# Optimization experiments

Measured on AMD Instinct MI355X. Metric: run time of the kernel, lower is better.

The kernel has to match this reference:

```python
import jax, jax.numpy as jnp
import numpy as np

D = 768      # feature_dim
HD = 768     # hidden_dim
NH = 4       # num_heads
B, T1, T2 = 4, 128, 128
LN_EPS = 1e-5

def setup_inputs() -> dict:
    key = jax.random.key(0)
    ks = jax.random.split(key, 12)
    s = 0.02
    return {
        'speech_features': jax.random.normal(ks[0], (B, T1, D), jnp.float32),
        'phoneme_features': jax.random.normal(ks[1], (B, T2, D), jnp.float32),
        # per-head attention MLP: Linear(2D->HD), ReLU, Linear(HD->1); stacked over heads
        'W1': jax.random.normal(ks[2], (NH, 2 * D, HD), jnp.float32) * s,
        'b1': jnp.zeros((NH, HD), jnp.float32),
        'w2': jax.random.normal(ks[3], (NH, HD), jnp.float32) * s,
        'b2': jnp.zeros((NH,), jnp.float32),
        # fusion: Linear(2D->2HD), ReLU, Linear(2HD->D), LayerNorm(D)
        'Wf1': jax.random.normal(ks[4], (2 * D, 2 * HD), jnp.float32) * s,
        'bf1': jnp.zeros((2 * HD,), jnp.float32),
        'Wf2': jax.random.normal(ks[5], (2 * HD, D), jnp.float32) * s,
        'bf2': jnp.zeros((D,), jnp.float32),
        'ln_g': jnp.ones((D,), jnp.float32),
        'ln_b': jnp.zeros((D,), jnp.float32),
    }

def reference(speech_features, phoneme_features, W1, b1, w2, b2, Wf1, bf1, Wf2, bf2, ln_g, ln_b):
    d = speech_features.shape[-1]
    # Decompose Linear(cat([speech_t, phoneme])) = speech@W1[:d] + phoneme@W1[d:] + b1
    Wx, Wy = W1[:, :d, :], W1[:, d:, :]
    sx = jnp.einsum('btd,ndh->nbth', speech_features, Wx)   # [NH,B,T1,HD]
    py = jnp.einsum('bsd,ndh->nbsh', phoneme_features, Wy)  # [NH,B,T2,HD]
    hidden = jax.nn.relu(sx[:, :, :, None, :] + py[:, :, None, :, :]
                         + b1[:, None, None, None, :])      # [NH,B,T1,T2,HD]
    scores = jnp.einsum('nbtsh,nh->nbts', hidden, w2) + b2[:, None, None, None]
    attn = jax.nn.softmax(scores, axis=-1).mean(axis=0)     # [B,T1,T2]
    context = jnp.einsum('bts,bsd->btd', attn, phoneme_features)  # [B,T1,D]
    fused = jnp.concatenate([speech_features, context], axis=-1)  # [B,T1,2D]
    # dropout is identity in eval mode
    h = jax.nn.relu(fused @ Wf1 + bf1)
    out = h @ Wf2 + bf2
    mu = out.mean(axis=-1, keepdims=True)
    var = ((out - mu) ** 2).mean(axis=-1, keepdims=True)
    out = (out - mu) * jax.lax.rsqrt(var + LN_EPS) * ln_g + ln_b
    return out.mean(axis=1)  # [B,D]
```

## Files before the change

kernel.cpp:

```cpp
#include <hip/hip_runtime.h>
#include <cstddef>


#define D_  768
#define HD_ 768
#define NH_ 4
#define B_  4
#define T1_ 128
#define T2_ 128
#define M_  (B_*T1_)
#define LN_EPS_ 1e-5f

typedef unsigned short u16;
typedef unsigned int u32;
typedef _Float16 f16;
typedef _Float16 f16x2 __attribute__((ext_vector_type(2)));
typedef __bf16 bf16x8 __attribute__((ext_vector_type(8)));
typedef float f32x4 __attribute__((ext_vector_type(4)));

__device__ __forceinline__ u16 f2bf(float f) {
    union { float f; unsigned int u; } v; v.f = f;
    unsigned int u = v.u + (0x7FFFu + ((v.u >> 16) & 1u));
    return (u16)(u >> 16);
}
__device__ __forceinline__ u16 f16bits(f16 h) {
    return __builtin_bit_cast(unsigned short, h);
}
__device__ __forceinline__ u32 splat2(u16 h) {
    return (u32)h * 0x10001u;
}
__device__ __forceinline__ u32 pk_add(u32 a, u32 b) {
    u32 d; asm("v_pk_add_f16 %0, %1, %2" : "=v"(d) : "v"(a), "v"(b)); return d;
}
__device__ __forceinline__ u32 pk_max0(u32 a) {
    u32 d; asm("v_pk_max_f16 %0, %1, %2" : "=v"(d) : "v"(a), "v"(0u)); return d;
}
__device__ __forceinline__ u32 pk_fma(u32 a, u32 b, u32 c) {
    u32 d; asm("v_pk_fma_f16 %0, %1, %2, %3" : "=v"(d) : "v"(a), "v"(b), "v"(c)); return d;
}
__device__ __forceinline__ float lo_f(u32 u) {
    f16x2 v = __builtin_bit_cast(f16x2, u); return (float)v.x;
}
__device__ __forceinline__ float hi_f(u32 u) {
    f16x2 v = __builtin_bit_cast(f16x2, u); return (float)v.y;
}

template<bool RELU, int MODE>
__device__ __forceinline__ void gemm_mfma_body(
    const u16* __restrict__ A, int lda,
    const u16* __restrict__ Bt, int ldb,
    const float* __restrict__ bias,
    void* __restrict__ C, int ldc, int K, int m0, int n0)
{
    __shared__ __align__(16) u16 As[64][40];
    __shared__ __align__(16) u16 Bs[64][40];
    __shared__ u16 Ts[MODE == 3 ? 64 : 1][MODE == 3 ? 68 : 1];

    const int tid = threadIdx.x;
    const int row = tid >> 2;
    const int kq  = (tid & 3) << 3;
    const int lane = tid & 63;
    const int w  = tid >> 6;
    const int wr = (w >> 1) << 5;
    const int wc = (w & 1) << 5;
    const int l16 = lane & 15;
    const int lk8 = (lane >> 4) << 3;
    const int r4  = (lane >> 4) << 2;

    const u16* aptr = A + (size_t)(m0 + row) * lda + kq;
    const u16* bptr = Bt + (size_t)(n0 + row) * ldb + kq;

    f32x4 acc00 = {0.f,0.f,0.f,0.f}, acc01 = {0.f,0.f,0.f,0.f};
    f32x4 acc10 = {0.f,0.f,0.f,0.f}, acc11 = {0.f,0.f,0.f,0.f};

    uint4 a_nxt = *(const uint4*)aptr;
    uint4 b_nxt = *(const uint4*)bptr;

    for (int k0 = 0; k0 < K; k0 += 32) {
        __syncthreads();
        *(uint4*)&As[row][kq] = a_nxt;
        *(uint4*)&Bs[row][kq] = b_nxt;
        if (k0 + 32 < K) {
            a_nxt = *(const uint4*)(aptr + k0 + 32);
            b_nxt = *(const uint4*)(bptr + k0 + 32);
        }
        __syncthreads();
        bf16x8 af0 = *(const bf16x8*)&As[wr + l16][lk8];
        bf16x8 af1 = *(const bf16x8*)&As[wr + 16 + l16][lk8];
        bf16x8 bf0 = *(const bf16x8*)&Bs[wc + l16][lk8];
        bf16x8 bf1 = *(const bf16x8*)&Bs[wc + 16 + l16][lk8];
        acc00 = __builtin_amdgcn_mfma_f32_16x16x32_bf16(af0, bf0, acc00, 0, 0, 0);
        acc01 = __builtin_amdgcn_mfma_f32_16x16x32_bf16(af0, bf1, acc01, 0, 0, 0);
        acc10 = __builtin_amdgcn_mfma_f32_16x16x32_bf16(af1, bf0, acc10, 0, 0, 0);
        acc11 = __builtin_amdgcn_mfma_f32_16x16x32_bf16(af1, bf1, acc11, 0, 0, 0);
    }

#define EPI_FRAG(ACC, MF, NF)                                                  \
    {                                                                          \
        const int gcol = n0 + wc + (NF)*16 + l16;                              \
        const float bv = bias ? bias[gcol] : 0.f;                              \
        float v_[4];                                                           \
        _Pragma("unroll")                                                      \
        for (int r = 0; r < 4; r++) {                                          \
            float v = ACC[r] + bv;                                             \
            if (RELU) v = fmaxf(v, 0.f);                                       \
            v_[r] = v;                                                         \
        }                                                                      \
        const int lr0 = wr + (MF)*16 + r4;                                     \
        if (MODE == 3) {                                                       \
            const int lc = wc + (NF)*16 + l16;                                 \
            _Pragma("unroll")                                                  \
            for (int r = 0; r < 4; r++) Ts[lc][lr0 + r] = f16bits((f16)v_[r]); \
        } else {                                                               \
            _Pragma("unroll")                                                  \
            for (int r = 0; r < 4; r++) {                                      \
                const size_t off = (size_t)(m0 + lr0 + r) * ldc + gcol;        \
                if (MODE == 0) ((float*)C)[off] = v_[r];                       \
                else if (MODE == 1) ((u16*)C)[off] = f2bf(v_[r]);              \
                else ((u16*)C)[off] = f16bits((f16)v_[r]);                     \
            }                                                                  \
        }                                                                      \
    }
    EPI_FRAG(acc00, 0, 0) EPI_FRAG(acc01, 0, 1)
    EPI_FRAG(acc10, 1, 0) EPI_FRAG(acc11, 1, 1)
#undef EPI_FRAG

    if (MODE == 3) {
        __syncthreads();
        u16* cb = (u16*)C + (size_t)(m0 >> 7) * (768 * 128) + (m0 & 127);
#pragma unroll
        for (int u = 0; u < 4; u++) {
            const int i = tid + u * 256;
            const int hl = i >> 4;
            const int s4 = (i & 15) << 2;
            ushort4 o;
            o.x = Ts[hl][s4 + 0]; o.y = Ts[hl][s4 + 1];
            o.z = Ts[hl][s4 + 2]; o.w = Ts[hl][s4 + 3];
            *(ushort4*)(cb + (size_t)(n0 + hl) * 128 + s4) = o;
        }
    }
}

__global__ __launch_bounds__(256) void prep_kernel(
    const float* __restrict__ speech, const float* __restrict__ phon,
    const float* __restrict__ W1, const float* __restrict__ Wf1,
    const float* __restrict__ Wf2,
    u16* __restrict__ spb, u16* __restrict__ phb,
    u16* __restrict__ w1t, u16* __restrict__ wf1t, u16* __restrict__ wf2t)
{
    const int tid = threadIdx.x;
    int bid = blockIdx.x;
    if (bid < 768) {
        const bool isp = bid < 384;
        const float* in = isp ? speech : phon;
        u16* outb = isp ? spb : phb;
        const int i = ((isp ? bid : bid - 384) * 256 + tid) * 4;
        float4 v = *(const float4*)(in + i);
        ushort4 o;
        o.x = f2bf(v.x); o.y = f2bf(v.y); o.z = f2bf(v.z); o.w = f2bf(v.w);
        *(ushort4*)(outb + i) = o;
        return;
    }
    bid -= 768;
    const float* in; u16* outp; int tx, ty;
    if (bid < 4608) {
        const int z = bid / 1152, r = bid % 1152;
        tx = r % 24; ty = r / 24;
        in = W1 + (size_t)z * 1536 * 768; outp = w1t + (size_t)z * 768 * 1536;
    } else if (bid < 6912) {
        const int r = bid - 4608;
        tx = r % 48; ty = r / 48;
        in = Wf1; outp = wf1t;
    } else {
        const int r = bid - 6912;
        tx = r % 24; ty = r / 24;
        in = Wf2; outp = wf2t;
    }
    const int C = (bid >= 4608 && bid < 6912) ? 1536 : 768;
    const int c0 = tx * 32, r0 = ty * 32;
    __shared__ float tile[32][33];
    const int tr = tid >> 3, tc = (tid & 7) << 2;
    float4 v = *(const float4*)(in + (size_t)(r0 + tr) * C + c0 + tc);
    tile[tr][tc] = v.x; tile[tr][tc + 1] = v.y; tile[tr][tc + 2] = v.z; tile[tr][tc + 3] = v.w;
    __syncthreads();
    ushort4 o;
    o.x = f2bf(tile[tc + 0][tr]); o.y = f2bf(tile[tc + 1][tr]);
    o.z = f2bf(tile[tc + 2][tr]); o.w = f2bf(tile[tc + 3][tr]);
    *(ushort4*)(outp + (size_t)(c0 + tr) * 1536 + r0 + tc) = o;
}

__global__ __launch_bounds__(256) void gemm_sxpy_kernel(
    const u16* __restrict__ sp, const u16* __restrict__ ph,
    const u16* __restrict__ w1t, const float* __restrict__ b1,
    u16* __restrict__ sxf, u16* __restrict__ pyt)
{
    const int z = blockIdx.z;
    const int n = z & 3;
    const bool ispy = z >= 4;
    const u16* Bt = w1t + (size_t)n * 768 * 1536 + (ispy ? 768 : 0);
    if (!ispy) {
        gemm_mfma_body<false, 2>(sp, 768, Bt, 1536, b1 + n * HD_,
                                 sxf + (size_t)n * M_ * HD_, HD_, 768,
                                 blockIdx.y * 64, blockIdx.x * 64);
    } else {
        gemm_mfma_body<false, 3>(ph, 768, Bt, 1536, nullptr,
                                 pyt + (size_t)n * 4 * 768 * 128, 0, 768,
                                 blockIdx.y * 64, blockIdx.x * 64);
    }
}

template<bool RELU, int MODE>
__global__ __launch_bounds__(256) void gemm_mfma_kernel(
    const u16* __restrict__ A, int lda,
    const u16* __restrict__ Bt, int ldb,
    const float* __restrict__ bias,
    void* __restrict__ C, int ldc, int K)
{
    gemm_mfma_body<RELU, MODE>(A, lda, Bt, ldb, bias, C, ldc, K,
                               blockIdx.y * 64, blockIdx.x * 64);
}

__global__ __launch_bounds__(256) void scores_softmax_kernel(
    const u16* __restrict__ sxf,
    const u16* __restrict__ pyt,
    const float* __restrict__ w2,
    float* __restrict__ probs)
{
    const int bid = blockIdx.x;
    const int n = bid >> 6, b = (bid >> 4) & 3, t0 = (bid & 15) * 8;
    const int tid = threadIdx.x, lane = tid & 63, w = tid >> 6;

    __shared__ __align__(16) u32 sxs[8][768];
    __shared__ __align__(16) u32 w2s[768];

    for (int q = 0; q < 6; q++) {
        const int u = tid + q * 256;
        const int r = u / 192;
        const int h4 = (u % 192) * 4;
        ushort4 v = *(const ushort4*)(sxf + ((size_t)(n * 512 + b * 128 + t0 + r)) * 768 + h4);
        sxs[r][h4 + 0] = splat2(v.x);
        sxs[r][h4 + 1] = splat2(v.y);
        sxs[r][h4 + 2] = splat2(v.z);
        sxs[r][h4 + 3] = splat2(v.w);
    }
    for (int q = 0; q < 3; q++) {
        const int i = tid + q * 256;
        w2s[i] = splat2(f16bits((f16)w2[n * 768 + i]));
    }
    __syncthreads();

    const u32* pypanel = (const u32*)(pyt + ((size_t)((n << 2) | b)) * 768 * 128) + lane;

    float accA0 = 0.f, accA1 = 0.f, accB0 = 0.f, accB1 = 0.f;
    const int rA = 2 * w, rB = 2 * w + 1;

    u32 b0[16], b1[16];
#pragma unroll
    for (int j = 0; j < 16; j++) b0[j] = pypanel[(size_t)j * 64];
#pragma unroll
    for (int j = 0; j < 16; j++) b1[j] = pypanel[(size_t)(16 + j) * 64];

    auto compute = [&](const u32 (&buf)[16], int hbase) {
        u32 aA = 0u, aB = 0u;
#pragma unroll
        for (int j = 0; j < 16; j++) {
            const u32 p = buf[j];
            const u32 wj = w2s[hbase + j];
            aA = pk_fma(pk_max0(pk_add(sxs[rA][hbase + j], p)), wj, aA);
            aB = pk_fma(pk_max0(pk_add(sxs[rB][hbase + j], p)), wj, aB);
        }
        accA0 += lo_f(aA); accA1 += hi_f(aA);
        accB0 += lo_f(aB); accB1 += hi_f(aB);
    };

    for (int hc = 0; hc < 768; hc += 32) {
        compute(b0, hc);
        if (hc + 32 < 768) {
#pragma unroll
            for (int j = 0; j < 16; j++) b0[j] = pypanel[(size_t)(hc + 32 + j) * 64];
        }
        compute(b1, hc + 16);
        if (hc + 48 < 768) {
#pragma unroll
            for (int j = 0; j < 16; j++) b1[j] = pypanel[(size_t)(hc + 48 + j) * 64];
        }
    }

#pragma unroll
    for (int which = 0; which < 2; which++) {
        const float s0 = which ? accB0 : accA0;
        const float s1 = which ? accB1 : accA1;
        const int t = t0 + 2 * w + which;
        float mx = fmaxf(s0, s1);
#pragma unroll
        for (int off = 32; off; off >>= 1) mx = fmaxf(mx, __shfl_xor(mx, off, 64));
        const float e0 = expf(s0 - mx), e1 = expf(s1 - mx);
        float sm = e0 + e1;
#pragma unroll
        for (int off = 32; off; off >>= 1) sm += __shfl_xor(sm, off, 64);
        const float inv = 0.25f / sm;
        float2 pr; pr.x = e0 * inv; pr.y = e1 * inv;
        *(float2*)&probs[((size_t)(n * 512 + b * 128 + t)) * 128 + 2 * lane] = pr;
    }
}

__global__ __launch_bounds__(256) void context_fused_kernel(
    const float* __restrict__ probs, const float* __restrict__ phon,
    const float* __restrict__ speech, u16* __restrict__ fused)
{
    const int m = blockIdx.x;
    const int b = m >> 7;
    const int tid = threadIdx.x;
    __shared__ float attn[T2_];
    if (tid < T2_) {
        float a = 0.f;
#pragma unroll
        for (int n = 0; n < NH_; n++)
            a += probs[(size_t)(n * M_ + m) * T2_ + tid];
        attn[tid] = a;
    }
    __syncthreads();
    const float* ph = phon + (size_t)b * T2_ * D_;
#pragma unroll
    for (int j = 0; j < 3; j++) {
        const int d = tid + 256 * j;
        float acc = 0.f;
#pragma unroll 8
        for (int s = 0; s < T2_; s++)
            acc = fmaf(attn[s], ph[(size_t)s * D_ + d], acc);
        fused[(size_t)m * (2 * D_) + d] = f2bf(speech[(size_t)m * D_ + d]);
        fused[(size_t)m * (2 * D_) + D_ + d] = f2bf(acc);
    }
}

__global__ __launch_bounds__(256) void ln_fused_kernel(
    const float* __restrict__ x, const float* __restrict__ g,
    const float* __restrict__ lb, float* __restrict__ out)
{
    const int b = blockIdx.x, tid = threadIdx.x, lane = tid & 63, w = tid >> 6;
    __shared__ float rs[T1_];
    __shared__ float Sred[4];

    float prsum = 0.f;
    for (int i = 0; i < 32; i++) {
        const int row = w * 32 + i;
        const float4* x4 = (const float4*)(x + ((size_t)(b * T1_ + row)) * D_);
        float s = 0.f, ss = 0.f;
#pragma unroll
        for (int j = 0; j < 3; j++) {
            float4 v = x4[j * 64 + lane];
            s += v.x + v.y + v.z + v.w;
            ss += v.x * v.x + v.y * v.y + v.z * v.z + v.w * v.w;
        }
#pragma unroll
        for (int off = 32; off; off >>= 1) {
            s += __shfl_xor(s, off, 64);
            ss += __shfl_xor(ss, off, 64);
        }
        if (lane == 0) {
            const float mu = s * (1.f / D_);
            const float var = ss * (1.f / D_) - mu * mu;
            const float r = rsqrtf(var + LN_EPS_);
            rs[row] = r;
            prsum += mu * r;
        }
    }
    if (lane == 0) Sred[w] = prsum;
    __syncthreads();
    const float S = Sred[0] + Sred[1] + Sred[2] + Sred[3];
    const float* xb = x + (size_t)b * T1_ * D_;
#pragma unroll
    for (int j = 0; j < 3; j++) {
        const int d = tid + 256 * j;
        float acc = 0.f;
#pragma unroll 8
        for (int t = 0; t < T1_; t++)
            acc = fmaf(xb[(size_t)t * D_ + d], rs[t], acc);
        out[b * D_ + d] = g[d] * (acc - S) * (1.f / T1_) + lb[d];
    }
}

extern "C" void kernel_launch(void* const* d_in, const int* in_sizes, int n_in,
                              void* d_out, int out_size, void* d_ws, size_t ws_size,
                              hipStream_t stream)
{
    const float* speech = (const float*)d_in[0];
    const float* phon   = (const float*)d_in[1];
    const float* W1     = (const float*)d_in[2];
    const float* b1     = (const float*)d_in[3];
    const float* w2     = (const float*)d_in[4];
    const float* Wf1    = (const float*)d_in[6];
    const float* bf1    = (const float*)d_in[7];
    const float* Wf2    = (const float*)d_in[8];
    const float* bf2    = (const float*)d_in[9];
    const float* ln_g   = (const float*)d_in[10];
    const float* ln_b   = (const float*)d_in[11];
    float* out = (float*)d_out;

    char* w = (char*)d_ws;
    auto alloc = [&](size_t bytes) { char* p = w; w += (bytes + 1023) & ~(size_t)1023; return p; };
    u16* sp_bf  = (u16*)alloc((size_t)M_ * D_ * 2);
    u16* ph_bf  = (u16*)alloc((size_t)M_ * D_ * 2);
    u16* w1t    = (u16*)alloc((size_t)NH_ * 768 * 1536 * 2);
    u16* wf1t   = (u16*)alloc((size_t)1536 * 1536 * 2);
    u16* wf2t   = (u16*)alloc((size_t)768 * 1536 * 2);
    u16* sxf    = (u16*)alloc((size_t)NH_ * M_ * HD_ * 2);
    u16* pyt    = (u16*)alloc((size_t)NH_ * B_ * 768 * 128 * 2);
    float* probs  = (float*)alloc((size_t)NH_ * M_ * T2_ * 4);
    u16* fusedb = (u16*)alloc((size_t)M_ * 2 * D_ * 2);
    u16* hbuf   = (u16*)alloc((size_t)M_ * 2 * HD_ * 2);
    float* outpre = (float*)alloc((size_t)M_ * D_ * 4);

    hipLaunchKernelGGL(prep_kernel, dim3(8832), dim3(256), 0, stream,
                       speech, phon, W1, Wf1, Wf2, sp_bf, ph_bf, w1t, wf1t, wf2t);
    hipLaunchKernelGGL(gemm_sxpy_kernel, dim3(HD_ / 64, M_ / 64, 8), dim3(256), 0, stream,
                       sp_bf, ph_bf, w1t, b1, sxf, pyt);
    hipLaunchKernelGGL(scores_softmax_kernel, dim3(256), dim3(256), 0, stream,
                       sxf, pyt, w2, probs);
    hipLaunchKernelGGL(context_fused_kernel, dim3(M_), dim3(256), 0, stream,
                       probs, phon, speech, fusedb);
    hipLaunchKernelGGL((gemm_mfma_kernel<true, 1>), dim3(2 * HD_ / 64, M_ / 64), dim3(256), 0, stream,
                       fusedb, 2 * D_, wf1t, 1536, bf1, hbuf, 2 * HD_, 2 * D_);
    hipLaunchKernelGGL((gemm_mfma_kernel<false, 0>), dim3(D_ / 64, M_ / 64), dim3(256), 0, stream,
                       hbuf, 2 * HD_, wf2t, 1536, bf2, outpre, D_, 2 * HD_);
    hipLaunchKernelGGL(ln_fused_kernel, dim3(B_), dim3(256), 0, stream,
                       outpre, ln_g, ln_b, out);
}
```

Baseline: 141.6 us.

## Give each wave one query row in scores kernel and use vector f16 builtins

The scores/softmax kernel now gives each wave one speech row instead of two, doubling the grid from 256 to 512 blocks and halving the shared staging of sx rows. The inline-asm packed f16 ops are replaced with compiler vector builtins, and the accumulator is split into four independent f16x2 chains that are folded into fp32 every 32 hidden units. This aims to raise occupancy and instruction-level parallelism on 256 CUs. In exchange, each py panel load now feeds only one row, so global and L2 traffic for pyt doubles.

```diff
diff --git a/kernel.cpp b/kernel.cpp
--- a/kernel.cpp
+++ b/kernel.cpp
@@ -26,24 +26,10 @@
 __device__ __forceinline__ u16 f16bits(f16 h) {
     return __builtin_bit_cast(unsigned short, h);
 }
-__device__ __forceinline__ u32 splat2(u16 h) {
-    return (u32)h * 0x10001u;
-}
-__device__ __forceinline__ u32 pk_add(u32 a, u32 b) {
-    u32 d; asm("v_pk_add_f16 %0, %1, %2" : "=v"(d) : "v"(a), "v"(b)); return d;
-}
-__device__ __forceinline__ u32 pk_max0(u32 a) {
-    u32 d; asm("v_pk_max_f16 %0, %1, %2" : "=v"(d) : "v"(a), "v"(0u)); return d;
-}
-__device__ __forceinline__ u32 pk_fma(u32 a, u32 b, u32 c) {
-    u32 d; asm("v_pk_fma_f16 %0, %1, %2, %3" : "=v"(d) : "v"(a), "v"(b), "v"(c)); return d;
-}
-__device__ __forceinline__ float lo_f(u32 u) {
-    f16x2 v = __builtin_bit_cast(f16x2, u); return (float)v.x;
-}
-__device__ __forceinline__ float hi_f(u32 u) {
-    f16x2 v = __builtin_bit_cast(f16x2, u); return (float)v.y;
-}
+__device__ __forceinline__ f16x2 bcast2(u32 u) {
+    return __builtin_bit_cast(f16x2, u);
+}
+__device__ __forceinline__ u32 splat2(u16 h) { return (u32)h * 0x10001u; }
 
 template<bool RELU, int MODE>
 __device__ __forceinline__ void gemm_mfma_body(
@@ -181,7 +167,8 @@
     __shared__ float tile[32][33];
     const int tr = tid >> 3, tc = (tid & 7) << 2;
     float4 v = *(const float4*)(in + (size_t)(r0 + tr) * C + c0 + tc);
-    tile[tr][tc] = v.x; tile[tr][tc + 1] = v.y; tile[tr][tc + 2] = v.z; tile[tr][tc + 3] = v.w;
+    tile[tr][tc] = v.x; tile[tr][tc + 1] = v.y;
+    tile[tr][tc + 2] = v.z; tile[tr][tc + 3] = v.w;
     __syncthreads();
     ushort4 o;
     o.x = f2bf(tile[tc + 0][tr]); o.y = f2bf(tile[tc + 1][tr]);
@@ -227,81 +214,78 @@
     float* __restrict__ probs)
 {
     const int bid = blockIdx.x;
-    const int n = bid >> 6, b = (bid >> 4) & 3, t0 = (bid & 15) * 8;
+    const int n = bid >> 7, b = (bid >> 5) & 3, t0 = (bid & 31) * 4;
     const int tid = threadIdx.x, lane = tid & 63, w = tid >> 6;
 
-    __shared__ __align__(16) u32 sxs[8][768];
-    __shared__ __align__(16) u32 w2s[768];
-
-    for (int q = 0; q < 6; q++) {
+    __shared__ __align__(16) f16x2 sxs[4][768];
+    __shared__ __align__(16) f16x2 w2s[768];
+
+#pragma unroll
+    for (int q = 0; q < 3; q++) {
         const int u = tid + q * 256;
         const int r = u / 192;
         const int h4 = (u % 192) * 4;
         ushort4 v = *(const ushort4*)(sxf + ((size_t)(n * 512 + b * 128 + t0 + r)) * 768 + h4);
-        sxs[r][h4 + 0] = splat2(v.x);
-        sxs[r][h4 + 1] = splat2(v.y);
-        sxs[r][h4 + 2] = splat2(v.z);
-        sxs[r][h4 + 3] = splat2(v.w);
-    }
+        sxs[r][h4 + 0] = bcast2(splat2(v.x));
+        sxs[r][h4 + 1] = bcast2(splat2(v.y));
+        sxs[r][h4 + 2] = bcast2(splat2(v.z));
+        sxs[r][h4 + 3] = bcast2(splat2(v.w));
+    }
+#pragma unroll
     for (int q = 0; q < 3; q++) {
         const int i = tid + q * 256;
-        w2s[i] = splat2(f16bits((f16)w2[n * 768 + i]));
+        w2s[i] = bcast2(splat2(f16bits((f16)w2[n * 768 + i])));
     }
     __syncthreads();
 
-    const u32* pypanel = (const u32*)(pyt + ((size_t)((n << 2) | b)) * 768 * 128) + lane;
-
-    float accA0 = 0.f, accA1 = 0.f, accB0 = 0.f, accB1 = 0.f;
-    const int rA = 2 * w, rB = 2 * w + 1;
-
-    u32 b0[16], b1[16];
+    const f16x2* pypanel = (const f16x2*)(pyt + ((size_t)((n << 2) | b)) * 768 * 128) + lane;
+    const f16x2 z2 = {(f16)0, (f16)0};
+
+    float acc0 = 0.f, acc1 = 0.f;
+
+    f16x2 b0[16], b1[16];
 #pragma unroll
     for (int j = 0; j < 16; j++) b0[j] = pypanel[(size_t)j * 64];
 #pragma unroll
     for (int j = 0; j < 16; j++) b1[j] = pypanel[(size_t)(16 + j) * 64];
 
-    auto compute = [&](const u32 (&buf)[16], int hbase) {
-        u32 aA = 0u, aB = 0u;
+    for (int hc = 0; hc < 768; hc += 32) {
+        f16x2 a4[4] = {z2, z2, z2, z2};
 #pragma unroll
         for (int j = 0; j < 16; j++) {
-            const u32 p = buf[j];
-            const u32 wj = w2s[hbase + j];
-            aA = pk_fma(pk_max0(pk_add(sxs[rA][hbase + j], p)), wj, aA);
-            aB = pk_fma(pk_max0(pk_add(sxs[rB][hbase + j], p)), wj, aB);
-        }
-        accA0 += lo_f(aA); accA1 += hi_f(aA);
-        accB0 += lo_f(aB); accB1 += hi_f(aB);
-    };
-
-    for (int hc = 0; hc < 768; hc += 32) {
-        compute(b0, hc);
+            f16x2 r_ = __builtin_elementwise_max(sxs[w][hc + j] + b0[j], z2);
+            a4[j & 3] = __builtin_elementwise_fma(r_, w2s[hc + j], a4[j & 3]);
+        }
         if (hc + 32 < 768) {
 #pragma unroll
             for (int j = 0; j < 16; j++) b0[j] = pypanel[(size_t)(hc + 32 + j) * 64];
         }
-        compute(b1, hc + 16);
+#pragma unroll
+        for (int j = 0; j < 16; j++) {
+            f16x2 r_ = __builtin_elementwise_max(sxs[w][hc + 16 + j] + b1[j], z2);
+            a4[j & 3] = __builtin_elementwise_fma(r_, w2s[hc + 16 + j], a4[j & 3]);
+        }
         if (hc + 48 < 768) {
 #pragma unroll
             for (int j = 0; j < 16; j++) b1[j] = pypanel[(size_t)(hc + 48 + j) * 64];
         }
-    }
-
-#pragma unroll
-    for (int which = 0; which < 2; which++) {
-        const float s0 = which ? accB0 : accA0;
-        const float s1 = which ? accB1 : accA1;
-        const int t = t0 + 2 * w + which;
-        float mx = fmaxf(s0, s1);
-#pragma unroll
-        for (int off = 32; off; off >>= 1) mx = fmaxf(mx, __shfl_xor(mx, off, 64));
-        const float e0 = expf(s0 - mx), e1 = expf(s1 - mx);
-        float sm = e0 + e1;
-#pragma unroll
-        for (int off = 32; off; off >>= 1) sm += __shfl_xor(sm, off, 64);
-        const float inv = 0.25f / sm;
-        float2 pr; pr.x = e0 * inv; pr.y = e1 * inv;
-        *(float2*)&probs[((size_t)(n * 512 + b * 128 + t)) * 128 + 2 * lane] = pr;
-    }
+#pragma unroll
+        for (int k = 0; k < 4; k++) {
+            acc0 += (float)a4[k].x;
+            acc1 += (float)a4[k].y;
+        }
+    }
+
+    float mx = fmaxf(acc0, acc1);
+#pragma unroll
+    for (int off = 32; off; off >>= 1) mx = fmaxf(mx, __shfl_xor(mx, off, 64));
+    const float e0 = expf(acc0 - mx), e1 = expf(acc1 - mx);
+    float sm = e0 + e1;
+#pragma unroll
+    for (int off = 32; off; off >>= 1) sm += __shfl_xor(sm, off, 64);
+    const float inv = 0.25f / sm;
+    float2 pr; pr.x = e0 * inv; pr.y = e1 * inv;
+    *(float2*)&probs[((size_t)(n * 512 + b * 128 + t0 + w)) * 128 + 2 * lane] = pr;
 }
 
 __global__ __launch_bounds__(256) void context_fused_kernel(
@@ -415,7 +399,7 @@
                        speech, phon, W1, Wf1, Wf2, sp_bf, ph_bf, w1t, wf1t, wf2t);
     hipLaunchKernelGGL(gemm_sxpy_kernel, dim3(HD_ / 64, M_ / 64, 8), dim3(256), 0, stream,
                        sp_bf, ph_bf, w1t, b1, sxf, pyt);
-    hipLaunchKernelGGL(scores_softmax_kernel, dim3(256), dim3(256), 0, stream,
+    hipLaunchKernelGGL(scores_softmax_kernel, dim3(512), dim3(256), 0, stream,
                        sxf, pyt, w2, probs);
     hipLaunchKernelGGL(context_fused_kernel, dim3(M_), dim3(256), 0, stream,
                        probs, phon, speech, fusedb);
```

After: 134.8 us. 1.05x faster.
